# Performance work log

Hardware: AMD Instinct MI355X
Metric: run time of the kernel (lower is better)

## Reference

```python
import jax, jax.numpy as jnp
import numpy as np

EMBED = 1024
HEADS = 16
DK = EMBED // HEADS


def setup_inputs() -> dict:
    key = jax.random.key(0)
    ks = jax.random.split(key, 6)
    B, S = 2, 2048
    scale = 1.0 / np.sqrt(EMBED)
    x = jax.random.normal(ks[0], (B, S, EMBED), dtype=jnp.float32)
    Wq = jax.random.normal(ks[1], (EMBED, EMBED), dtype=jnp.float32) * scale
    Wk = jax.random.normal(ks[2], (EMBED, EMBED), dtype=jnp.float32) * scale
    Wv = jax.random.normal(ks[3], (EMBED, EMBED), dtype=jnp.float32) * scale
    Wo = jax.random.normal(ks[4], (EMBED, EMBED), dtype=jnp.float32) * scale
    qw = jnp.zeros((HEADS, 1), dtype=jnp.float32)  # quantum_weight, init quantum_scale=0
    return {"x": x, "Wq": Wq, "Wk": Wk, "Wv": Wv, "Wo": Wo, "qw": qw}


def reference(x, Wq, Wk, Wv, Wo, qw):
    B, S, E = x.shape
    # nn.Linear with no bias: y = x @ W.T; split heads -> [B,H,S,Dk]
    def proj(W):
        return (x @ W.T).reshape(B, S, HEADS, DK).transpose(0, 2, 1, 3)
    q, k, v = proj(Wq), proj(Wk), proj(Wv)
    scores = jnp.einsum('bhsd,bhtd->bhst', q, k) / np.sqrt(DK)
    attn = jax.nn.softmax(scores, axis=-1)  # dropout in eval mode: identity
    classical = jnp.einsum('bhst,bhtd->bhsd', attn, v)
    w = jax.nn.sigmoid(qw)[:, :, None]  # [H,1,1] per-head mixing weight
    out = w * jnp.sin(classical) + (1.0 - w) * classical
    out = out.transpose(0, 2, 1, 3).reshape(B, S, E)
    return out @ Wo.T
```

## Files before the change

### kernel.cpp

```cpp
#include <hip/hip_runtime.h>
#include <math.h>

constexpr int Ec  = 1024;
constexpr int Hc  = 16;
constexpr int DKc = 64;
constexpr int Bc  = 2;
constexpr int Sc  = 2048;
constexpr int Mc  = Bc * Sc;

typedef _Float16 half8 __attribute__((ext_vector_type(8)));
typedef _Float16 half4 __attribute__((ext_vector_type(4)));
typedef float    floatx4  __attribute__((ext_vector_type(4)));
typedef float    floatx16 __attribute__((ext_vector_type(16)));
typedef unsigned int uint2v __attribute__((ext_vector_type(2)));
typedef unsigned int uint4v __attribute__((ext_vector_type(4)));

#define MFMA16(a, b, c) __builtin_amdgcn_mfma_f32_16x16x32_f16(a, b, c, 0, 0, 0)
#define MFMA32(a, b, c) __builtin_amdgcn_mfma_f32_32x32x16_f16(a, b, c, 0, 0, 0)

__device__ __forceinline__ void async_lds16(const _Float16* g, _Float16* l)
{
    __builtin_amdgcn_global_load_lds(
        (const __attribute__((address_space(1))) unsigned int*)g,
        (__attribute__((address_space(3))) unsigned int*)l, 16, 0, 0);
}

__device__ __forceinline__ unsigned pkh2(float a, float b)
{
    return __builtin_bit_cast(unsigned, __builtin_amdgcn_cvt_pkrtz(a, b));
}

__global__ __launch_bounds__(256)
void convert_to_h(const float4* __restrict__ x,
                  const float4* __restrict__ wq,
                  const float4* __restrict__ wk,
                  const float4* __restrict__ wv,
                  const float4* __restrict__ wo,
                  half4* __restrict__ dst)
{
    const int i = blockIdx.x * 256 + threadIdx.x;
    const float4* src; int off;
    if      (i < 1048576) { src = x;  off = i; }
    else if (i < 1310720) { src = wq; off = i - 1048576; }
    else if (i < 1572864) { src = wk; off = i - 1310720; }
    else if (i < 1835008) { src = wv; off = i - 1572864; }
    else                  { src = wo; off = i - 1835008; }
    const float4 v = src[off];
    half4 o;
    o.x = (_Float16)v.x; o.y = (_Float16)v.y;
    o.z = (_Float16)v.z; o.w = (_Float16)v.w;
    dst[i] = o;
}

__device__ __forceinline__ void mfma_gemm_core64(const _Float16* __restrict__ A,
                                                 const _Float16* __restrict__ Bw,
                                                 int m0, int n0,
                                                 _Float16* As, _Float16* Bs,
                                                 floatx4 acc[4][4])
{
    const int tid  = threadIdx.x;
    const int wave = tid >> 6, lane = tid & 63;
    const int l16  = lane & 15, quad = lane >> 4;
    const int wrow = (wave >> 1) * 64, wcol = (wave & 1) * 64;

    const int srow8  = lane >> 3;
    const int schunk = (lane & 7) ^ (srow8 & 7);
    const _Float16* ga = A  + (size_t)(m0 + wave * 32 + srow8) * Ec + schunk * 8;
    const _Float16* gb = Bw + (size_t)(n0 + wave * 32 + srow8) * Ec + schunk * 8;
    _Float16* lA = As + (size_t)(wave * 32) * 64;
    _Float16* lB = Bs + (size_t)(wave * 32) * 64;

    for (int kt = 0; kt < Ec; kt += 64) {
#pragma unroll
        for (int c = 0; c < 4; ++c) {
            async_lds16(ga + (size_t)(c * 8) * Ec + kt, lA + c * 512);
            async_lds16(gb + (size_t)(c * 8) * Ec + kt, lB + c * 512);
        }
        __syncthreads();

        half8 af[4][2], bf[4][2];
#pragma unroll
        for (int i = 0; i < 4; ++i) {
            const int ra = wrow + i * 16 + l16;
            const int rb = wcol + i * 16 + l16;
#pragma unroll
            for (int kc = 0; kc < 2; ++kc) {
                af[i][kc] = *(const half8*)&As[ra * 64 + (((quad + kc * 4) ^ (ra & 7)) * 8)];
                bf[i][kc] = *(const half8*)&Bs[rb * 64 + (((quad + kc * 4) ^ (rb & 7)) * 8)];
            }
        }
#pragma unroll
        for (int i = 0; i < 4; ++i)
#pragma unroll
            for (int j = 0; j < 4; ++j) {
                acc[i][j] = MFMA16(af[i][0], bf[j][0], acc[i][j]);
                acc[i][j] = MFMA16(af[i][1], bf[j][1], acc[i][j]);
            }
        __syncthreads();
    }
}

__global__ __launch_bounds__(256)
void gemm_qkv_mfma(const _Float16* __restrict__ xh,
                   const _Float16* __restrict__ wqh,
                   const _Float16* __restrict__ wkh,
                   const _Float16* __restrict__ wvh,
                   _Float16* __restrict__ Qh,
                   _Float16* __restrict__ Kh,
                   _Float16* __restrict__ VTh)
{
    __shared__ __align__(16) _Float16 As[128 * 64];
    __shared__ __align__(16) _Float16 Bs[128 * 64];
    const int z = blockIdx.z;
    const _Float16* W = (z == 0) ? wqh : (z == 1) ? wkh : wvh;
    const int m0 = blockIdx.y * 128, n0 = blockIdx.x * 128;

    floatx4 acc[4][4] = {};
    mfma_gemm_core64(xh, W, m0, n0, As, Bs, acc);

    const int tid  = threadIdx.x;
    const int wave = tid >> 6, lane = tid & 63;
    const int l16  = lane & 15, quad = lane >> 4;
    const int wrow = (wave >> 1) * 64, wcol = (wave & 1) * 64;

    if (z == 2) {
#pragma unroll
        for (int i = 0; i < 4; ++i)
#pragma unroll
            for (int j = 0; j < 4; ++j) {
                const int n  = n0 + wcol + j * 16 + l16;
                const int hh = n >> 6, d = n & 63;
                const int mb = m0 + wrow + i * 16 + quad * 4;
                const int bb = mb >> 11, s = mb & (Sc - 1);
                half4 pk;
#pragma unroll
                for (int r = 0; r < 4; ++r) pk[r] = (_Float16)acc[i][j][r];
                *(half4*)&VTh[((size_t)((bb * Hc + hh) * DKc + d)) * Sc + s] = pk;
            }
    } else {
        _Float16* out = (z == 0) ? Qh : Kh;
        const float scale = (z == 0) ? 0.18033688011112042f : 1.0f;
#pragma unroll
        for (int i = 0; i < 4; ++i)
#pragma unroll
            for (int j = 0; j < 4; ++j) {
                const int n = n0 + wcol + j * 16 + l16;
#pragma unroll
                for (int r = 0; r < 4; ++r) {
                    const int m = m0 + wrow + i * 16 + quad * 4 + r;
                    out[(size_t)m * Ec + n] = (_Float16)(acc[i][j][r] * scale);
                }
            }
    }
}

__global__ __launch_bounds__(256)
void gemm_out_mfma(const _Float16* __restrict__ A,
                   const _Float16* __restrict__ W,
                   float* __restrict__ C)
{
    __shared__ __align__(16) _Float16 As[128 * 64];
    __shared__ __align__(16) _Float16 Bs[64 * 64];
    const int m0 = blockIdx.y * 128, n0 = blockIdx.x * 64;

    const int tid  = threadIdx.x;
    const int wave = tid >> 6, lane = tid & 63;
    const int l16  = lane & 15, quad = lane >> 4;
    const int wrow = (wave >> 1) * 64, wcol = (wave & 1) * 32;

    const int srow8  = lane >> 3;
    const int schunk = (lane & 7) ^ (srow8 & 7);
    const _Float16* ga = A + (size_t)(m0 + wave * 32 + srow8) * Ec + schunk * 8;
    const _Float16* gb = W + (size_t)(n0 + wave * 16 + srow8) * Ec + schunk * 8;
    _Float16* lA = As + (size_t)(wave * 32) * 64;
    _Float16* lB = Bs + (size_t)(wave * 16) * 64;

    floatx4 acc[4][2] = {};

    for (int kt = 0; kt < Ec; kt += 64) {
#pragma unroll
        for (int c = 0; c < 4; ++c)
            async_lds16(ga + (size_t)(c * 8) * Ec + kt, lA + c * 512);
#pragma unroll
        for (int c = 0; c < 2; ++c)
            async_lds16(gb + (size_t)(c * 8) * Ec + kt, lB + c * 512);
        __syncthreads();

        half8 af[4][2], bf[2][2];
#pragma unroll
        for (int i = 0; i < 4; ++i) {
            const int ra = wrow + i * 16 + l16;
#pragma unroll
            for (int kc = 0; kc < 2; ++kc)
                af[i][kc] = *(const half8*)&As[ra * 64 + (((quad + kc * 4) ^ (ra & 7)) * 8)];
        }
#pragma unroll
        for (int j = 0; j < 2; ++j) {
            const int rb = wcol + j * 16 + l16;
#pragma unroll
            for (int kc = 0; kc < 2; ++kc)
                bf[j][kc] = *(const half8*)&Bs[rb * 64 + (((quad + kc * 4) ^ (rb & 7)) * 8)];
        }
#pragma unroll
        for (int i = 0; i < 4; ++i)
#pragma unroll
            for (int j = 0; j < 2; ++j) {
                acc[i][j] = MFMA16(af[i][0], bf[j][0], acc[i][j]);
                acc[i][j] = MFMA16(af[i][1], bf[j][1], acc[i][j]);
            }
        __syncthreads();
    }

#pragma unroll
    for (int i = 0; i < 4; ++i)
#pragma unroll
        for (int j = 0; j < 2; ++j) {
            const int n = n0 + wcol + j * 16 + l16;
#pragma unroll
            for (int r = 0; r < 4; ++r) {
                const int m = m0 + wrow + i * 16 + quad * 4 + r;
                C[(size_t)m * Ec + n] = acc[i][j][r];
            }
        }
}

__global__ __launch_bounds__(512, 4)
void flash_attn(const _Float16* __restrict__ Qh,
                const _Float16* __restrict__ Kh,
                const _Float16* __restrict__ VTh,
                const float* __restrict__ qw,
                _Float16* __restrict__ Mixh)
{
    constexpr int BM = 128, BN = 64;
    constexpr int NT = (Sc / BN) / 2;
    __shared__ __align__(16) _Float16 KV[2][2][2][64 * 64];
    __shared__ float Ls[2][128];

    const int tid  = threadIdx.x;
    const int g    = tid >> 8;
    const int wl   = (tid >> 6) & 3;
    const int lane = tid & 63;
    const int l31  = lane & 31, hi = lane >> 5;
    const int q0 = blockIdx.x * BM;
    const int bh = blockIdx.y;
    const int h  = bh & (Hc - 1), b = bh >> 4;

    half8 aq[4];
    {
        const _Float16* qp = Qh + (size_t)(b * Sc + q0 + wl * 32 + l31) * Ec
                                + h * DKc + hi * 8;
#pragma unroll
        for (int ks = 0; ks < 4; ++ks) aq[ks] = *(const half8*)(qp + ks * 16);
    }

    const int srow   = lane >> 3;
    const int schunk = (lane & 7) ^ srow;
    const _Float16* Kg = Kh + (size_t)(b * Sc + g * (Sc / 2) + wl * 16 + srow) * Ec
                            + h * DKc + schunk * 8;
    const _Float16* Vg = VTh + ((size_t)(bh * DKc + wl * 16 + srow)) * Sc
                             + g * (Sc / 2) + schunk * 8;

    floatx16 o[2] = {};
    float l_run = 0.f;
    const int xk = l31 & 7;

    {
        _Float16* kb = KV[g][0][0] + (wl * 16) * 64;
        _Float16* vb = KV[g][0][1] + (wl * 16) * 64;
        async_lds16(Kg, kb);
        async_lds16(Kg + (size_t)8 * Ec, kb + 8 * 64);
        async_lds16(Vg, vb);
        async_lds16(Vg + (size_t)8 * Sc, vb + 8 * 64);
    }
    __syncthreads();

    int cur = 0;
    for (int n = 0; n < NT; ++n) {
        if (n + 1 < NT) {
            _Float16* kb = KV[g][cur ^ 1][0] + (wl * 16) * 64;
            _Float16* vb = KV[g][cur ^ 1][1] + (wl * 16) * 64;
            const _Float16* kg = Kg + (size_t)(n + 1) * BN * Ec;
            const _Float16* vg = Vg + (size_t)(n + 1) * BN;
            async_lds16(kg, kb);
            async_lds16(kg + (size_t)8 * Ec, kb + 8 * 64);
            async_lds16(vg, vb);
            async_lds16(vg + (size_t)8 * Sc, vb + 8 * 64);
        }
        const _Float16* Kb = KV[g][cur][0];
        const _Float16* Vb = KV[g][cur][1];

#pragma unroll
        for (int t = 0; t < 2; ++t) {
            floatx16 st = {};
#pragma unroll
            for (int ks = 0; ks < 4; ++ks) {
                const half8 ak = *(const half8*)
                    (Kb + (t * 32 + l31) * 64 + ((((ks << 1) | hi) ^ xk) << 3));
                st = MFMA32(ak, aq[ks], st);
            }
            float p[16];
#pragma unroll
            for (int r = 0; r < 16; ++r) p[r] = __builtin_amdgcn_exp2f(st[r]);
#pragma unroll
            for (int r = 0; r < 16; ++r) l_run += p[r];
            half8 pa[2];
#pragma unroll
            for (int e = 0; e < 2; ++e) {
                const unsigned X0 = pkh2(p[8 * e + 0], p[8 * e + 1]);
                const unsigned X1 = pkh2(p[8 * e + 2], p[8 * e + 3]);
                const unsigned Y0 = pkh2(p[8 * e + 4], p[8 * e + 5]);
                const unsigned Y1 = pkh2(p[8 * e + 6], p[8 * e + 7]);
                const uint2v s0 = __builtin_amdgcn_permlane32_swap(X0, Y0, false, false);
                const uint2v s1 = __builtin_amdgcn_permlane32_swap(X1, Y1, false, false);
                uint4v w;
                w.x = s0.x; w.y = s1.x; w.z = s0.y; w.w = s1.y;
                pa[e] = __builtin_bit_cast(half8, w);
            }
#pragma unroll
            for (int dt = 0; dt < 2; ++dt)
#pragma unroll
                for (int e = 0; e < 2; ++e) {
                    const int ks = 2 * t + e;
                    const half8 bv = *(const half8*)
                        (Vb + (dt * 32 + l31) * 64 + ((((ks << 1) | hi) ^ xk) << 3));
                    o[dt] = MFMA32(pa[e], bv, o[dt]);
                }
        }
        __syncthreads();
        cur ^= 1;
    }

    l_run += __shfl_xor(l_run, 32);
    if (hi == 0) Ls[g][wl * 32 + l31] = l_run;

    float* Os = (float*)&KV[0][0][0][0];
    if (g == 1) {
#pragma unroll
        for (int dt = 0; dt < 2; ++dt)
#pragma unroll
            for (int r = 0; r < 16; ++r) {
                const int row = wl * 32 + (r & 3) + 8 * (r >> 2) + 4 * hi;
                Os[row * 66 + dt * 32 + l31] = o[dt][r];
            }
    }
    __syncthreads();
    if (g == 0) {
        const float wmix = 1.f / (1.f + __expf(-qw[h]));
#pragma unroll
        for (int r = 0; r < 16; ++r) {
            const int row = wl * 32 + (r & 3) + 8 * (r >> 2) + 4 * hi;
            const float inv = 1.f / (Ls[0][row] + Ls[1][row]);
            _Float16* mp = Mixh + (size_t)(b * Sc + q0 + row) * Ec + h * DKc;
#pragma unroll
            for (int dt = 0; dt < 2; ++dt) {
                const float v = (o[dt][r] + Os[row * 66 + dt * 32 + l31]) * inv;
                mp[dt * 32 + l31] = (_Float16)(wmix * __sinf(v) + (1.f - wmix) * v);
            }
        }
    }
}

extern "C" void kernel_launch(void* const* d_in, const int* in_sizes, int n_in,
                              void* d_out, int out_size, void* d_ws, size_t ws_size,
                              hipStream_t stream)
{
    const float* x  = (const float*)d_in[0];
    const float* Wq = (const float*)d_in[1];
    const float* Wk = (const float*)d_in[2];
    const float* Wv = (const float*)d_in[3];
    const float* Wo = (const float*)d_in[4];
    const float* qw = (const float*)d_in[5];
    float* out = (float*)d_out;

    _Float16* hb   = (_Float16*)d_ws;
    _Float16* xh   = hb;
    _Float16* wqh  = hb + (size_t)4 * 1024 * 1024;
    _Float16* wkh  = hb + (size_t)5 * 1024 * 1024;
    _Float16* wvh  = hb + (size_t)6 * 1024 * 1024;
    _Float16* woh  = hb + (size_t)7 * 1024 * 1024;
    _Float16* Qh   = hb + (size_t)8 * 1024 * 1024;
    _Float16* Kh   = hb + (size_t)12 * 1024 * 1024;
    _Float16* VTh  = hb + (size_t)16 * 1024 * 1024;
    _Float16* mixh = hb + (size_t)20 * 1024 * 1024;

    convert_to_h<<<dim3(8192), dim3(256), 0, stream>>>(
        (const float4*)x, (const float4*)Wq, (const float4*)Wk,
        (const float4*)Wv, (const float4*)Wo, (half4*)hb);

    gemm_qkv_mfma<<<dim3(Ec / 128, Mc / 128, 3), dim3(256), 0, stream>>>(
        xh, wqh, wkh, wvh, Qh, Kh, VTh);

    flash_attn<<<dim3(Sc / 128, Bc * Hc), dim3(512), 0, stream>>>(
        Qh, Kh, VTh, qw, mixh);

    gemm_out_mfma<<<dim3(Ec / 64, Mc / 128), dim3(256), 0, stream>>>(
        mixh, woh, out);
}
```

Before: 188.8 us.

## Swizzle GEMM block order, fuse QKV weights, unroll attention double-buffer with setprio

Measured after the change: 189.7 us. No clear change (+0.5%).

```diff
diff --git a/kernel.cpp b/kernel.cpp
--- a/kernel.cpp
+++ b/kernel.cpp
@@ -101,34 +101,36 @@
 }
 
 __global__ __launch_bounds__(256)
-void gemm_qkv_mfma(const _Float16* __restrict__ xh,
-                   const _Float16* __restrict__ wqh,
-                   const _Float16* __restrict__ wkh,
-                   const _Float16* __restrict__ wvh,
-                   _Float16* __restrict__ Qh,
-                   _Float16* __restrict__ Kh,
-                   _Float16* __restrict__ VTh)
+void gemm_qkv_fused(const _Float16* __restrict__ xh,
+                    const _Float16* __restrict__ wall,
+                    _Float16* __restrict__ Qh,
+                    _Float16* __restrict__ Kh,
+                    _Float16* __restrict__ VTh)
 {
     __shared__ __align__(16) _Float16 As[128 * 64];
     __shared__ __align__(16) _Float16 Bs[128 * 64];
-    const int z = blockIdx.z;
-    const _Float16* W = (z == 0) ? wqh : (z == 1) ? wkh : wvh;
-    const int m0 = blockIdx.y * 128, n0 = blockIdx.x * 128;
+    const int lin = blockIdx.x;
+    const int swz = (lin & 7) * 96 + (lin >> 3);
+    const int m0  = (swz / 24) * 128;
+    const int n0f = (swz % 24) * 128;
 
     floatx4 acc[4][4] = {};
-    mfma_gemm_core64(xh, W, m0, n0, As, Bs, acc);
+    mfma_gemm_core64(xh, wall, m0, n0f, As, Bs, acc);
 
     const int tid  = threadIdx.x;
     const int wave = tid >> 6, lane = tid & 63;
     const int l16  = lane & 15, quad = lane >> 4;
     const int wrow = (wave >> 1) * 64, wcol = (wave & 1) * 64;
 
+    const int z   = n0f >> 10;
+    const int nl0 = n0f & 1023;
+
     if (z == 2) {
 #pragma unroll
         for (int i = 0; i < 4; ++i)
 #pragma unroll
             for (int j = 0; j < 4; ++j) {
-                const int n  = n0 + wcol + j * 16 + l16;
+                const int n  = nl0 + wcol + j * 16 + l16;
                 const int hh = n >> 6, d = n & 63;
                 const int mb = m0 + wrow + i * 16 + quad * 4;
                 const int bb = mb >> 11, s = mb & (Sc - 1);
@@ -144,7 +146,7 @@
         for (int i = 0; i < 4; ++i)
 #pragma unroll
             for (int j = 0; j < 4; ++j) {
-                const int n = n0 + wcol + j * 16 + l16;
+                const int n = nl0 + wcol + j * 16 + l16;
 #pragma unroll
                 for (int r = 0; r < 4; ++r) {
                     const int m = m0 + wrow + i * 16 + quad * 4 + r;
@@ -161,7 +163,9 @@
 {
     __shared__ __align__(16) _Float16 As[128 * 64];
     __shared__ __align__(16) _Float16 Bs[64 * 64];
-    const int m0 = blockIdx.y * 128, n0 = blockIdx.x * 64;
+    const int lin = blockIdx.x;
+    const int swz = (lin & 7) * 64 + (lin >> 3);
+    const int m0 = (swz >> 4) * 128, n0 = (swz & 15) * 64;
 
     const int tid  = threadIdx.x;
     const int wave = tid >> 6, lane = tid & 63;
@@ -260,75 +264,98 @@
     const _Float16* Vg = VTh + ((size_t)(bh * DKc + wl * 16 + srow)) * Sc
                              + g * (Sc / 2) + schunk * 8;
 
+    const int xk = l31 & 7;
+    const _Float16* kbase[4];
+    const _Float16* vbase[4];
+#pragma unroll
+    for (int ks = 0; ks < 4; ++ks) {
+        const int xo = ((((ks << 1) | hi) ^ xk) << 3);
+        kbase[ks] = KV[g][0][0] + l31 * 64 + xo;
+        vbase[ks] = KV[g][0][1] + l31 * 64 + xo;
+    }
+    _Float16* kd0 = KV[g][0][0] + (wl * 16) * 64;
+    _Float16* vd0 = KV[g][0][1] + (wl * 16) * 64;
+
     floatx16 o[2] = {};
     float l_run = 0.f;
-    const int xk = l31 & 7;
-
-    {
-        _Float16* kb = KV[g][0][0] + (wl * 16) * 64;
-        _Float16* vb = KV[g][0][1] + (wl * 16) * 64;
-        async_lds16(Kg, kb);
-        async_lds16(Kg + (size_t)8 * Ec, kb + 8 * 64);
-        async_lds16(Vg, vb);
-        async_lds16(Vg + (size_t)8 * Sc, vb + 8 * 64);
-    }
+
+    async_lds16(Kg, kd0);
+    async_lds16(Kg + (size_t)8 * Ec, kd0 + 512);
+    async_lds16(Vg, vd0);
+    async_lds16(Vg + (size_t)8 * Sc, vd0 + 512);
     __syncthreads();
 
-    int cur = 0;
-    for (int n = 0; n < NT; ++n) {
-        if (n + 1 < NT) {
-            _Float16* kb = KV[g][cur ^ 1][0] + (wl * 16) * 64;
-            _Float16* vb = KV[g][cur ^ 1][1] + (wl * 16) * 64;
-            const _Float16* kg = Kg + (size_t)(n + 1) * BN * Ec;
-            const _Float16* vg = Vg + (size_t)(n + 1) * BN;
-            async_lds16(kg, kb);
-            async_lds16(kg + (size_t)8 * Ec, kb + 8 * 64);
-            async_lds16(vg, vb);
-            async_lds16(vg + (size_t)8 * Sc, vb + 8 * 64);
-        }
-        const _Float16* Kb = KV[g][cur][0];
-        const _Float16* Vb = KV[g][cur][1];
-
-#pragma unroll
-        for (int t = 0; t < 2; ++t) {
-            floatx16 st = {};
-#pragma unroll
-            for (int ks = 0; ks < 4; ++ks) {
-                const half8 ak = *(const half8*)
-                    (Kb + (t * 32 + l31) * 64 + ((((ks << 1) | hi) ^ xk) << 3));
-                st = MFMA32(ak, aq[ks], st);
-            }
-            float p[16];
-#pragma unroll
-            for (int r = 0; r < 16; ++r) p[r] = __builtin_amdgcn_exp2f(st[r]);
-#pragma unroll
-            for (int r = 0; r < 16; ++r) l_run += p[r];
-            half8 pa[2];
-#pragma unroll
-            for (int e = 0; e < 2; ++e) {
-                const unsigned X0 = pkh2(p[8 * e + 0], p[8 * e + 1]);
-                const unsigned X1 = pkh2(p[8 * e + 2], p[8 * e + 3]);
-                const unsigned Y0 = pkh2(p[8 * e + 4], p[8 * e + 5]);
-                const unsigned Y1 = pkh2(p[8 * e + 6], p[8 * e + 7]);
-                const uint2v s0 = __builtin_amdgcn_permlane32_swap(X0, Y0, false, false);
-                const uint2v s1 = __builtin_amdgcn_permlane32_swap(X1, Y1, false, false);
-                uint4v w;
-                w.x = s0.x; w.y = s1.x; w.z = s0.y; w.w = s1.y;
-                pa[e] = __builtin_bit_cast(half8, w);
-            }
-#pragma unroll
-            for (int dt = 0; dt < 2; ++dt)
-#pragma unroll
-                for (int e = 0; e < 2; ++e) {
-                    const int ks = 2 * t + e;
-                    const half8 bv = *(const half8*)
-                        (Vb + (dt * 32 + l31) * 64 + ((((ks << 1) | hi) ^ xk) << 3));
-                    o[dt] = MFMA32(pa[e], bv, o[dt]);
-                }
-        }
-        __syncthreads();
-        cur ^= 1;
-    }
+    const _Float16* kgp = Kg + (size_t)BN * Ec;
+    const _Float16* vgp = Vg + BN;
+
+#define ATTN_TILE(CO)                                                         \
+    {                                                                         \
+        _Pragma("unroll")                                                     \
+        for (int t = 0; t < 2; ++t) {                                         \
+            floatx16 st = {};                                                 \
+            __builtin_amdgcn_s_setprio(1);                                    \
+            _Pragma("unroll")                                                 \
+            for (int ks = 0; ks < 4; ++ks)                                    \
+                st = MFMA32(*(const half8*)(kbase[ks] + (CO) + t * 2048),     \
+                            aq[ks], st);                                      \
+            __builtin_amdgcn_s_setprio(0);                                    \
+            float p[16];                                                      \
+            _Pragma("unroll")                                                 \
+            for (int r = 0; r < 16; ++r) p[r] = __builtin_amdgcn_exp2f(st[r]);\
+            float s8[8];                                                      \
+            _Pragma("unroll")                                                 \
+            for (int r = 0; r < 8; ++r) s8[r] = p[2 * r] + p[2 * r + 1];      \
+            float s4[4];                                                      \
+            _Pragma("unroll")                                                 \
+            for (int r = 0; r < 4; ++r) s4[r] = s8[2 * r] + s8[2 * r + 1];    \
+            l_run += ((s4[0] + s4[1]) + (s4[2] + s4[3]));                     \
+            half8 pa[2];                                                      \
+            _Pragma("unroll")                                                 \
+            for (int e = 0; e < 2; ++e) {                                     \
+                const unsigned X0 = pkh2(p[8 * e + 0], p[8 * e + 1]);         \
+                const unsigned X1 = pkh2(p[8 * e + 2], p[8 * e + 3]);         \
+                const unsigned Y0 = pkh2(p[8 * e + 4], p[8 * e + 5]);         \
+                const unsigned Y1 = pkh2(p[8 * e + 6], p[8 * e + 7]);         \
+                const uint2v s0 = __builtin_amdgcn_permlane32_swap(X0, Y0, false, false); \
+                const uint2v s1 = __builtin_amdgcn_permlane32_swap(X1, Y1, false, false); \
+                uint4v w; w.x = s0.x; w.y = s1.x; w.z = s0.y; w.w = s1.y;     \
+                pa[e] = __builtin_bit_cast(half8, w);                         \
+            }                                                                 \
+            __builtin_amdgcn_s_setprio(1);                                    \
+            _Pragma("unroll")                                                 \
+            for (int dt = 0; dt < 2; ++dt)                                    \
+                _Pragma("unroll")                                             \
+                for (int e = 0; e < 2; ++e) {                                 \
+                    const half8 bv = *(const half8*)                          \
+                        (vbase[2 * t + e] + (CO) + dt * 2048);                \
+                    o[dt] = MFMA32(pa[e], bv, o[dt]);                         \
+                }                                                             \
+            __builtin_amdgcn_s_setprio(0);                                    \
+        }                                                                     \
+    }
+
+    for (int n = 0; n < NT; n += 2) {
+        async_lds16(kgp, kd0 + 8192);
+        async_lds16(kgp + (size_t)8 * Ec, kd0 + 8192 + 512);
+        async_lds16(vgp, vd0 + 8192);
+        async_lds16(vgp + (size_t)8 * Sc, vd0 + 8192 + 512);
+        kgp += (size_t)BN * Ec; vgp += BN;
+
+        ATTN_TILE(0)
+        __syncthreads();
+
+        if (n + 2 < NT) {
+            async_lds16(kgp, kd0);
+            async_lds16(kgp + (size_t)8 * Ec, kd0 + 512);
+            async_lds16(vgp, vd0);
+            async_lds16(vgp + (size_t)8 * Sc, vd0 + 512);
+            kgp += (size_t)BN * Ec; vgp += BN;
+        }
+
+        ATTN_TILE(8192)
+        __syncthreads();
+    }
+#undef ATTN_TILE
 
     l_run += __shfl_xor(l_run, 32);
     if (hi == 0) Ls[g][wl * 32 + l31] = l_run;
@@ -375,8 +402,6 @@
     _Float16* hb   = (_Float16*)d_ws;
     _Float16* xh   = hb;
     _Float16* wqh  = hb + (size_t)4 * 1024 * 1024;
-    _Float16* wkh  = hb + (size_t)5 * 1024 * 1024;
-    _Float16* wvh  = hb + (size_t)6 * 1024 * 1024;
     _Float16* woh  = hb + (size_t)7 * 1024 * 1024;
     _Float16* Qh   = hb + (size_t)8 * 1024 * 1024;
     _Float16* Kh   = hb + (size_t)12 * 1024 * 1024;
@@ -387,12 +412,12 @@
         (const float4*)x, (const float4*)Wq, (const float4*)Wk,
         (const float4*)Wv, (const float4*)Wo, (half4*)hb);
 
-    gemm_qkv_mfma<<<dim3(Ec / 128, Mc / 128, 3), dim3(256), 0, stream>>>(
-        xh, wqh, wkh, wvh, Qh, Kh, VTh);
+    gemm_qkv_fused<<<dim3(768), dim3(256), 0, stream>>>(
+        xh, wqh, Qh, Kh, VTh);
 
     flash_attn<<<dim3(Sc / 128, Bc * Hc), dim3(512), 0, stream>>>(
         Qh, Kh, VTh, qw, mixh);
 
-    gemm_out_mfma<<<dim3(Ec / 64, Mc / 128), dim3(256), 0, stream>>>(
+    gemm_out_mfma<<<dim3(512), dim3(256), 0, stream>>>(
         mixh, woh, out);
 }
```
